# Performance work log

Hardware: AMD Instinct MI355X
Metric: run time of the kernel (lower is better)

Reference implementation:

```python
import jax, jax.numpy as jnp
import numpy as np
from math import sqrt

DIM = 256
NUM_HEADS = 4
GROUPS = 32  # min(256//4, 32)
EPS = 1e-6


def group_norm(x, gamma, beta, groups=GROUPS, eps=EPS):
    # x: (B, C, H, W); normalize per group over (C//G, H, W)
    B, C, H, W = x.shape
    xg = x.reshape(B, groups, C // groups, H, W)
    mu = jnp.mean(xg, axis=(2, 3, 4), keepdims=True)
    var = jnp.var(xg, axis=(2, 3, 4), keepdims=True)
    xn = ((xg - mu) * jax.lax.rsqrt(var + eps)).reshape(B, C, H, W)
    return xn * gamma[None, :, None, None] + beta[None, :, None, None]


def lin_on_channel(x, W, bias):
    # torch Linear on channel dim: W is (out, in)
    return jnp.einsum('bchw,oc->bohw', x, W) + bias[None, :, None, None]


def setup_inputs() -> dict:
    key = jax.random.key(0)
    ks = jax.random.split(key, 14)
    B, C, H, W = 16, DIM, 32, 32
    s = 1.0 / sqrt(DIM)
    return {
        'a': jax.random.normal(ks[0], (B, C, H, W), jnp.float32),
        'b': jax.random.normal(ks[1], (B, C, H, W), jnp.float32),
        'Wq': jax.random.normal(ks[2], (DIM, DIM), jnp.float32) * s,
        'bq': jnp.zeros((DIM,), jnp.float32),
        'Wk': jax.random.normal(ks[3], (DIM, DIM), jnp.float32) * s,
        'bk': jnp.zeros((DIM,), jnp.float32),
        'Wv': jax.random.normal(ks[4], (DIM, DIM), jnp.float32) * s,
        'bv': jnp.zeros((DIM,), jnp.float32),
        'Wp': jax.random.normal(ks[5], (DIM, DIM), jnp.float32) * s,
        'bp': jnp.zeros((DIM,), jnp.float32),
        'gnA_w': jnp.ones((DIM,), jnp.float32),
        'gnA_b': jnp.zeros((DIM,), jnp.float32),
        'gnB_w': jnp.ones((DIM,), jnp.float32),
        'gnB_b': jnp.zeros((DIM,), jnp.float32),
    }


def reference(a, b, Wq, bq, Wk, bk, Wv, bv, Wp, bp, gnA_w, gnA_b, gnB_w, gnB_b):
    B, C, H, W = a.shape
    _, _, H2, W2 = b.shape
    dh = DIM // NUM_HEADS
    skip_b = b
    an = group_norm(a, gnA_w, gnA_b)
    bn = group_norm(b, gnB_w, gnB_b)
    q = lin_on_channel(bn, Wq, bq).reshape(B, NUM_HEADS, dh, H2, W2)
    k = lin_on_channel(an, Wk, bk).reshape(B, NUM_HEADS, dh, H, W)
    # NOTE: value uses pre-posemb but post-groupnorm 'a' (same as an here)
    v = lin_on_channel(an, Wv, bv).reshape(B, NUM_HEADS, dh, H, W)
    scores = jnp.einsum('bhdxy,bhdij->bhxyij', q, k) / sqrt(DIM)
    attn = jax.nn.softmax(scores.reshape(B, NUM_HEADS, H2, W2, H * W), axis=-1)
    attn = attn.reshape(B, NUM_HEADS, H2, W2, H, W)
    h = jnp.einsum('bhxyij,bhdij->bhdxy', attn, v).reshape(B, DIM, H2, W2)
    h = lin_on_channel(h, Wp, bp)
    ret = skip_b + h
    return ret / sqrt(2.0)
```

## Files before the change

### kernel.cpp

```cpp
#include <hip/hip_runtime.h>
#include <hip/hip_bf16.h>

#define BSZ 16
#define CDIM 256
#define NPIX 1024
#define NH 4
#define DHD 64
#define EPSV 1e-6f
#define QSCALE 0.0625f
#define INV_SQRT2 0.70710678118654752440f

typedef __attribute__((ext_vector_type(4))) float f32x4;
typedef __attribute__((ext_vector_type(8))) __bf16 bf16x8;
typedef __attribute__((ext_vector_type(4))) __bf16 bf16x4;

#define OFF_WBF   0UL
#define OFF_STATS (512UL*1024)
#define OFF_ANT   (1024UL*1024)
#define OFF_BNT   (OFF_ANT + 8UL*1024*1024)
#define OFF_Q     (OFF_BNT + 8UL*1024*1024)
#define OFF_K     (OFF_Q   + 8UL*1024*1024)
#define OFF_V     (OFF_K   + 8UL*1024*1024)
#define OFF_H     (OFF_V   + 8UL*1024*1024)

__global__ __launch_bounds__(256) void prep_w(const float* __restrict__ Wq, const float* __restrict__ Wk,
                                              const float* __restrict__ Wv, const float* __restrict__ Wp,
                                              __bf16* __restrict__ out){
  int m = blockIdx.y;
  const float* src = (m==0)?Wq:(m==1)?Wk:(m==2)?Wv:Wp;
  float scale = (m==0)?QSCALE:1.0f;
  int idx = (blockIdx.x*256 + threadIdx.x)*4;
  float4 v = *(const float4*)(src + idx);
  bf16x4 o;
  o[0]=(__bf16)(v.x*scale); o[1]=(__bf16)(v.y*scale);
  o[2]=(__bf16)(v.z*scale); o[3]=(__bf16)(v.w*scale);
  *(bf16x4*)(out + m*65536 + idx) = o;
}

__global__ __launch_bounds__(256) void gn_stats(const float* __restrict__ xa, const float* __restrict__ xb,
                                                float2* __restrict__ stats){
  int bx = blockIdx.x;
  int t = bx >> 9; int rem = bx & 511; int bb = rem >> 5; int g = rem & 31;
  const float* src = (t ? xb : xa) + ((size_t)(bb*CDIM + g*8))*NPIX;
  float s = 0.f, ss = 0.f;
  for (int i = 0; i < 8; i++){
    float4 v = *(const float4*)(src + (threadIdx.x + 256*i)*4);
    s  += v.x+v.y+v.z+v.w;
    ss += v.x*v.x+v.y*v.y+v.z*v.z+v.w*v.w;
  }
  __shared__ float rs[256], rss[256];
  rs[threadIdx.x]=s; rss[threadIdx.x]=ss; __syncthreads();
  for (int st=128; st>0; st>>=1){
    if (threadIdx.x < st){ rs[threadIdx.x]+=rs[threadIdx.x+st]; rss[threadIdx.x]+=rss[threadIdx.x+st]; }
    __syncthreads();
  }
  if (threadIdx.x==0){
    float mean = rs[0]*(1.0f/8192.0f);
    float var  = rss[0]*(1.0f/8192.0f) - mean*mean;
    stats[(t*16+bb)*32+g] = make_float2(mean, rsqrtf(var + EPSV));
  }
}

__global__ __launch_bounds__(256) void norm_t(const float* __restrict__ xa, const float* __restrict__ xb,
                                              const float* __restrict__ gAw, const float* __restrict__ gAb,
                                              const float* __restrict__ gBw, const float* __restrict__ gBb,
                                              const float2* __restrict__ stats,
                                              __bf16* __restrict__ ant, __bf16* __restrict__ bnt){
  __shared__ __align__(16) __bf16 T[64][72];
  int t = blockIdx.z;
  const float* src = t ? xb : xa;
  const float* gw  = t ? gBw : gAw;
  const float* gb  = t ? gBb : gAb;
  __bf16* dst = t ? bnt : ant;
  int bb = blockIdx.y >> 2, cblk = blockIdx.y & 3;
  int p0 = blockIdx.x*64, c0 = cblk*64;
  int tid = threadIdx.x;
  int r16 = tid>>4, c4 = tid&15;
  for (int pass=0; pass<4; pass++){
    int cl = r16 + 16*pass;
    int c  = c0 + cl;
    float2 ms = stats[(t*16+bb)*32 + (c>>3)];
    float sc  = ms.y * gw[c];
    float off = gb[c] - ms.x*sc;
    float4 v = *(const float4*)(src + ((size_t)(bb*CDIM + c))*NPIX + p0 + c4*4);
    T[c4*4+0][cl] = (__bf16)(v.x*sc+off);
    T[c4*4+1][cl] = (__bf16)(v.y*sc+off);
    T[c4*4+2][cl] = (__bf16)(v.z*sc+off);
    T[c4*4+3][cl] = (__bf16)(v.w*sc+off);
  }
  __syncthreads();
  for (int pass=0; pass<2; pass++){
    int slot = tid + 256*pass;
    int pl = slot>>3, ch = slot&7;
    *(float4*)(dst + ((size_t)(bb*NPIX + p0 + pl))*CDIM + c0 + ch*8) = *(float4*)&T[pl][ch*8];
  }
}

__global__ __launch_bounds__(256) void gemm_k(const __bf16* __restrict__ A, const __bf16* __restrict__ Bm,
                                              const float* __restrict__ bias, float bias_scale,
                                              void* __restrict__ dst_, const float* __restrict__ skip,
                                              int mode){
  __shared__ __align__(16) __bf16 As[64][72], Bs[64][72];
  int tid = threadIdx.x;
  int m0 = blockIdx.y*64, n0 = blockIdx.x*64;
  int lane = tid & 63, wid = tid >> 6;
  int wm = (wid>>1)*32, wn = (wid&1)*32;
  int g = lane>>4, c = lane&15;
  f32x4 acc[2][2];
  #pragma unroll
  for (int i=0;i<2;i++)
    #pragma unroll
    for (int j=0;j<2;j++) acc[i][j] = (f32x4){0.f,0.f,0.f,0.f};

  for (int k0=0; k0<256; k0+=64){
    #pragma unroll
    for (int i=0;i<2;i++){
      int slot = tid + 256*i;
      int row = slot>>3, ch = slot&7;
      *(float4*)&As[row][ch*8] = *(const float4*)(A  + (size_t)(m0+row)*256 + k0 + ch*8);
      *(float4*)&Bs[row][ch*8] = *(const float4*)(Bm + (size_t)(n0+row)*256 + k0 + ch*8);
    }
    __syncthreads();
    #pragma unroll
    for (int ks=0; ks<2; ks++){
      bf16x8 af0 = *(bf16x8*)&As[wm +      c][ks*32 + g*8];
      bf16x8 af1 = *(bf16x8*)&As[wm + 16 + c][ks*32 + g*8];
      bf16x8 bf0 = *(bf16x8*)&Bs[wn +      c][ks*32 + g*8];
      bf16x8 bf1 = *(bf16x8*)&Bs[wn + 16 + c][ks*32 + g*8];
      acc[0][0] = __builtin_amdgcn_mfma_f32_16x16x32_bf16(af0, bf0, acc[0][0], 0,0,0);
      acc[0][1] = __builtin_amdgcn_mfma_f32_16x16x32_bf16(af0, bf1, acc[0][1], 0,0,0);
      acc[1][0] = __builtin_amdgcn_mfma_f32_16x16x32_bf16(af1, bf0, acc[1][0], 0,0,0);
      acc[1][1] = __builtin_amdgcn_mfma_f32_16x16x32_bf16(af1, bf1, acc[1][1], 0,0,0);
    }
    __syncthreads();
  }

  #pragma unroll
  for (int fm=0; fm<2; fm++){
    #pragma unroll
    for (int fn=0; fn<2; fn++){
      int m = m0 + wm + fm*16 + g*4;
      int n = n0 + wn + fn*16 + c;
      f32x4 v = acc[fm][fn];
      if (mode <= 1){
        int bb = n>>10, p = n&1023;
        int o = m, h = o>>6, d = o&63;
        bf16x4 pk;
        #pragma unroll
        for (int r=0;r<4;r++) pk[r] = (__bf16)(v[r] + bias[o+r]*bias_scale);
        *(bf16x4*)((__bf16*)dst_ + ((size_t)((bb*4+h)*1024 + p))*64 + d) = pk;
      } else if (mode == 2){
        int bb = m>>10, p = m&1023;
        int o = n, h = o>>6, d = o&63;
        float bv = bias[o];
        bf16x4 pk;
        #pragma unroll
        for (int r=0;r<4;r++) pk[r] = (__bf16)(v[r] + bv);
        *(bf16x4*)((__bf16*)dst_ + ((size_t)((bb*4+h)*64 + d))*1024 + p) = pk;
      } else {
        int bb = m>>10, p = m&1023;
        int o = n;
        float bv = bias[o];
        size_t addr = (size_t)(bb*256 + o)*1024 + p;
        float4 sk = *(const float4*)(skip + addr);
        float4 ov;
        ov.x = (sk.x + v[0] + bv)*INV_SQRT2;
        ov.y = (sk.y + v[1] + bv)*INV_SQRT2;
        ov.z = (sk.z + v[2] + bv)*INV_SQRT2;
        ov.w = (sk.w + v[3] + bv)*INV_SQRT2;
        *(float4*)((float*)dst_ + addr) = ov;
      }
    }
  }
}

__global__ __launch_bounds__(256) void attn_k(const __bf16* __restrict__ q, const __bf16* __restrict__ k,
                                              const __bf16* __restrict__ v, __bf16* __restrict__ hout){
  __shared__ __align__(16) __bf16 Kl[64][72], Vl[64][72], Pl[4][16][72];
  __shared__ float l_lds[4][16];
  int bh = blockIdx.y;
  int qblk = blockIdx.x;
  int tid = threadIdx.x, lane = tid&63, w = tid>>6;
  int g = lane>>4, c = lane&15;
  int bb = bh>>2, h = bh&3;
  const __bf16* qbase = q + (size_t)bh*NPIX*DHD;
  const __bf16* kbase = k + (size_t)bh*NPIX*DHD;
  const __bf16* vbase = v + (size_t)bh*DHD*NPIX;

  int qrow = qblk*64 + w*16 + c;
  bf16x8 qf0 = *(const bf16x8*)(qbase + (size_t)qrow*64 +      g*8);
  bf16x8 qf1 = *(const bf16x8*)(qbase + (size_t)qrow*64 + 32 + g*8);

  f32x4 oacc[4];
  #pragma unroll
  for (int i=0;i<4;i++) oacc[i] = (f32x4){0.f,0.f,0.f,0.f};
  float l0=0.f, l1=0.f, l2=0.f, l3=0.f;

  for (int kt=0; kt<16; kt++){
    #pragma unroll
    for (int i=0;i<2;i++){
      int slot = tid + 256*i;
      int row = slot>>3, ch = slot&7;
      *(float4*)&Kl[row][ch*8] = *(const float4*)(kbase + (size_t)(kt*64+row)*64 + ch*8);
      *(float4*)&Vl[row][ch*8] = *(const float4*)(vbase + (size_t)row*1024 + kt*64 + ch*8);
    }
    __syncthreads();
    f32x4 s[4];
    #pragma unroll
    for (int fn=0; fn<4; fn++){
      bf16x8 kb0 = *(bf16x8*)&Kl[fn*16 + c][     g*8];
      bf16x8 kb1 = *(bf16x8*)&Kl[fn*16 + c][32 + g*8];
      f32x4 z = (f32x4){0.f,0.f,0.f,0.f};
      z     = __builtin_amdgcn_mfma_f32_16x16x32_bf16(qf0, kb0, z, 0,0,0);
      s[fn] = __builtin_amdgcn_mfma_f32_16x16x32_bf16(qf1, kb1, z, 0,0,0);
    }
    #pragma unroll
    for (int fn=0; fn<4; fn++){
      float p0 = __expf(s[fn][0]); l0 += p0; Pl[w][g*4+0][fn*16+c] = (__bf16)p0;
      float p1 = __expf(s[fn][1]); l1 += p1; Pl[w][g*4+1][fn*16+c] = (__bf16)p1;
      float p2 = __expf(s[fn][2]); l2 += p2; Pl[w][g*4+2][fn*16+c] = (__bf16)p2;
      float p3 = __expf(s[fn][3]); l3 += p3; Pl[w][g*4+3][fn*16+c] = (__bf16)p3;
    }
    bf16x8 pb0 = *(bf16x8*)&Pl[w][c][     g*8];
    bf16x8 pb1 = *(bf16x8*)&Pl[w][c][32 + g*8];
    #pragma unroll
    for (int fm=0; fm<4; fm++){
      bf16x8 va0 = *(bf16x8*)&Vl[fm*16+c][     g*8];
      bf16x8 va1 = *(bf16x8*)&Vl[fm*16+c][32 + g*8];
      oacc[fm] = __builtin_amdgcn_mfma_f32_16x16x32_bf16(va0, pb0, oacc[fm], 0,0,0);
      oacc[fm] = __builtin_amdgcn_mfma_f32_16x16x32_bf16(va1, pb1, oacc[fm], 0,0,0);
    }
    __syncthreads();
  }

  l0 += __shfl_xor(l0,1); l0 += __shfl_xor(l0,2); l0 += __shfl_xor(l0,4); l0 += __shfl_xor(l0,8);
  l1 += __shfl_xor(l1,1); l1 += __shfl_xor(l1,2); l1 += __shfl_xor(l1,4); l1 += __shfl_xor(l1,8);
  l2 += __shfl_xor(l2,1); l2 += __shfl_xor(l2,2); l2 += __shfl_xor(l2,4); l2 += __shfl_xor(l2,8);
  l3 += __shfl_xor(l3,1); l3 += __shfl_xor(l3,2); l3 += __shfl_xor(l3,4); l3 += __shfl_xor(l3,8);
  float lv = (c==0)?l0:(c==1)?l1:(c==2)?l2:l3;
  if (c < 4) l_lds[w][g*4+c] = lv;
  __syncthreads();
  float linv = 1.0f / l_lds[w][c];

  int qg = qblk*64 + w*16 + c;
  #pragma unroll
  for (int fm=0; fm<4; fm++){
    bf16x4 pk;
    #pragma unroll
    for (int r=0;r<4;r++) pk[r] = (__bf16)(oacc[fm][r]*linv);
    *(bf16x4*)(hout + ((size_t)(bb*NPIX + qg))*CDIM + h*64 + fm*16 + g*4) = pk;
  }
}

extern "C" void kernel_launch(void* const* d_in, const int* in_sizes, int n_in,
                              void* d_out, int out_size, void* d_ws, size_t ws_size,
                              hipStream_t stream) {
  const float* xa  = (const float*)d_in[0];
  const float* xb  = (const float*)d_in[1];
  const float* Wq  = (const float*)d_in[2];
  const float* bq  = (const float*)d_in[3];
  const float* Wk  = (const float*)d_in[4];
  const float* bk  = (const float*)d_in[5];
  const float* Wv  = (const float*)d_in[6];
  const float* bv  = (const float*)d_in[7];
  const float* Wp  = (const float*)d_in[8];
  const float* bp  = (const float*)d_in[9];
  const float* gAw = (const float*)d_in[10];
  const float* gAb = (const float*)d_in[11];
  const float* gBw = (const float*)d_in[12];
  const float* gBb = (const float*)d_in[13];

  char* ws = (char*)d_ws;
  __bf16* wbf   = (__bf16*)(ws + OFF_WBF);
  float2* stats = (float2*)(ws + OFF_STATS);
  __bf16* ant   = (__bf16*)(ws + OFF_ANT);
  __bf16* bnt   = (__bf16*)(ws + OFF_BNT);
  __bf16* qws   = (__bf16*)(ws + OFF_Q);
  __bf16* kws   = (__bf16*)(ws + OFF_K);
  __bf16* vws   = (__bf16*)(ws + OFF_V);
  __bf16* hws   = (__bf16*)(ws + OFF_H);

  prep_w<<<dim3(64,4), 256, 0, stream>>>(Wq, Wk, Wv, Wp, wbf);
  gn_stats<<<1024, 256, 0, stream>>>(xa, xb, stats);
  norm_t<<<dim3(16,64,2), 256, 0, stream>>>(xa, xb, gAw, gAb, gBw, gBb, stats, ant, bnt);
  gemm_k<<<dim3(256,4), 256, 0, stream>>>(wbf,           bnt, bq, QSCALE, qws, nullptr, 0);
  gemm_k<<<dim3(256,4), 256, 0, stream>>>(wbf + 65536,   ant, bk, 1.0f,   kws, nullptr, 0);
  gemm_k<<<dim3(4,256), 256, 0, stream>>>(ant, wbf + 2*65536, bv, 1.0f,   vws, nullptr, 2);
  attn_k<<<dim3(16,64), 256, 0, stream>>>(qws, kws, vws, hws);
  gemm_k<<<dim3(4,256), 256, 0, stream>>>(hws, wbf + 3*65536, bp, 1.0f, d_out, xb, 3);
}
```

Measured before the change: 195.7 us.

## Merge Q/K GEMMs, enlarge GEMM tiles, prefetch global loads, remap blocks for XCD locality

Q and K projections are merged into one 128x128-tiled GEMM launch, and the V and output projections use a 128x64 tile, so there are fewer launches and more reuse per block. All GEMMs and the attention kernel now prefetch the next K-tile into registers while computing the current one. Block indices are remapped with an (i0&7) swizzle, LDS row padding changes from 72 to 76, and s_setprio is raised around the MFMA sections in attention. The costs are higher register pressure and possibly lower occupancy from the larger tiles.

Measured after the change: 259.7 us. +32.7%, slower.

```diff
diff --git a/kernel.cpp b/kernel.cpp
--- a/kernel.cpp
+++ b/kernel.cpp
@@ -96,78 +96,158 @@
   }
 }
 
-__global__ __launch_bounds__(256) void gemm_k(const __bf16* __restrict__ A, const __bf16* __restrict__ Bm,
-                                              const float* __restrict__ bias, float bias_scale,
-                                              void* __restrict__ dst_, const float* __restrict__ skip,
-                                              int mode){
-  __shared__ __align__(16) __bf16 As[64][72], Bs[64][72];
-  int tid = threadIdx.x;
-  int m0 = blockIdx.y*64, n0 = blockIdx.x*64;
-  int lane = tid & 63, wid = tid >> 6;
-  int wm = (wid>>1)*32, wn = (wid&1)*32;
-  int g = lane>>4, c = lane&15;
-  f32x4 acc[2][2];
-  #pragma unroll
-  for (int i=0;i<2;i++)
-    #pragma unroll
-    for (int j=0;j<2;j++) acc[i][j] = (f32x4){0.f,0.f,0.f,0.f};
-
-  for (int k0=0; k0<256; k0+=64){
-    #pragma unroll
-    for (int i=0;i<2;i++){
-      int slot = tid + 256*i;
-      int row = slot>>3, ch = slot&7;
-      *(float4*)&As[row][ch*8] = *(const float4*)(A  + (size_t)(m0+row)*256 + k0 + ch*8);
-      *(float4*)&Bs[row][ch*8] = *(const float4*)(Bm + (size_t)(n0+row)*256 + k0 + ch*8);
-    }
-    __syncthreads();
-    #pragma unroll
-    for (int ks=0; ks<2; ks++){
-      bf16x8 af0 = *(bf16x8*)&As[wm +      c][ks*32 + g*8];
-      bf16x8 af1 = *(bf16x8*)&As[wm + 16 + c][ks*32 + g*8];
-      bf16x8 bf0 = *(bf16x8*)&Bs[wn +      c][ks*32 + g*8];
-      bf16x8 bf1 = *(bf16x8*)&Bs[wn + 16 + c][ks*32 + g*8];
-      acc[0][0] = __builtin_amdgcn_mfma_f32_16x16x32_bf16(af0, bf0, acc[0][0], 0,0,0);
-      acc[0][1] = __builtin_amdgcn_mfma_f32_16x16x32_bf16(af0, bf1, acc[0][1], 0,0,0);
-      acc[1][0] = __builtin_amdgcn_mfma_f32_16x16x32_bf16(af1, bf0, acc[1][0], 0,0,0);
-      acc[1][1] = __builtin_amdgcn_mfma_f32_16x16x32_bf16(af1, bf1, acc[1][1], 0,0,0);
-    }
-    __syncthreads();
-  }
-
-  #pragma unroll
-  for (int fm=0; fm<2; fm++){
-    #pragma unroll
-    for (int fn=0; fn<2; fn++){
+__global__ __launch_bounds__(256) void gemm_qk(const __bf16* __restrict__ Wqk,
+    const __bf16* __restrict__ bnt, const __bf16* __restrict__ ant,
+    const float* __restrict__ bq, const float* __restrict__ bk,
+    __bf16* __restrict__ qws, __bf16* __restrict__ kws){
+  __shared__ __align__(16) __bf16 As[128][76], Bs[128][76];
+  int i0 = blockIdx.x;
+  int wg = (i0&7)*64 + (i0>>3);
+  int my = wg&3, nx = wg>>2;
+  int m0 = my*128, n0 = nx*128;
+  const __bf16* Bm = (my<2) ? bnt : ant;
+  int tid=threadIdx.x, lane=tid&63, wid=tid>>6;
+  int wm=(wid>>1)*64, wn=(wid&1)*64, g=lane>>4, c=lane&15;
+  f32x4 acc[4][4];
+  #pragma unroll
+  for (int i=0;i<4;i++)
+    #pragma unroll
+    for (int j=0;j<4;j++) acc[i][j]=(f32x4){0.f,0.f,0.f,0.f};
+  int row[4], ch[4];
+  #pragma unroll
+  for (int i=0;i<4;i++){ int slot=tid+256*i; row[i]=slot>>3; ch[i]=slot&7; }
+  float4 rA[4], rB[4];
+  #pragma unroll
+  for (int i=0;i<4;i++){
+    rA[i] = *(const float4*)(Wqk + (size_t)(m0+row[i])*256 + ch[i]*8);
+    rB[i] = *(const float4*)(Bm  + (size_t)(n0+row[i])*256 + ch[i]*8);
+  }
+  #pragma unroll
+  for (int t=0;t<4;t++){
+    #pragma unroll
+    for (int i=0;i<4;i++){
+      *(float4*)&As[row[i]][ch[i]*8] = rA[i];
+      *(float4*)&Bs[row[i]][ch[i]*8] = rB[i];
+    }
+    __syncthreads();
+    if (t<3){
+      int k0=(t+1)*64;
+      #pragma unroll
+      for (int i=0;i<4;i++){
+        rA[i] = *(const float4*)(Wqk + (size_t)(m0+row[i])*256 + k0 + ch[i]*8);
+        rB[i] = *(const float4*)(Bm  + (size_t)(n0+row[i])*256 + k0 + ch[i]*8);
+      }
+    }
+    #pragma unroll
+    for (int ks=0;ks<2;ks++){
+      bf16x8 af[4], bfr[4];
+      #pragma unroll
+      for (int i=0;i<4;i++) af[i]  = *(bf16x8*)&As[wm+i*16+c][ks*32+g*8];
+      #pragma unroll
+      for (int j=0;j<4;j++) bfr[j] = *(bf16x8*)&Bs[wn+j*16+c][ks*32+g*8];
+      #pragma unroll
+      for (int i=0;i<4;i++)
+        #pragma unroll
+        for (int j=0;j<4;j++)
+          acc[i][j] = __builtin_amdgcn_mfma_f32_16x16x32_bf16(af[i], bfr[j], acc[i][j],0,0,0);
+    }
+    __syncthreads();
+  }
+  const float* bias = (my<2)? bq : bk;
+  float bscale = (my<2)? QSCALE : 1.0f;
+  __bf16* dst = (my<2)? qws : kws;
+  int mbase = (my<2)? m0 : (m0-256);
+  #pragma unroll
+  for (int fm=0;fm<4;fm++){
+    #pragma unroll
+    for (int fn=0;fn<4;fn++){
+      int o = mbase + wm + fm*16 + g*4;
+      int n = n0 + wn + fn*16 + c;
+      int bb=n>>10, p=n&1023;
+      f32x4 v = acc[fm][fn];
+      bf16x4 pk;
+      #pragma unroll
+      for (int r=0;r<4;r++) pk[r] = (__bf16)(v[r] + bias[o+r]*bscale);
+      *(bf16x4*)(dst + ((size_t)((bb*4+(o>>6))*1024 + p))*64 + (o&63)) = pk;
+    }
+  }
+}
+
+__global__ __launch_bounds__(256) void gemm_sw(const __bf16* __restrict__ A,
+    const __bf16* __restrict__ Wn, const float* __restrict__ bias,
+    void* __restrict__ dst_, const float* __restrict__ skip, int mode){
+  __shared__ __align__(16) __bf16 As[128][76], Bs[64][76];
+  int i0 = blockIdx.x;
+  int wg = (i0&7)*64 + (i0>>3);
+  int ny = wg&3, mx = wg>>2;
+  int m0 = mx*128, n0 = ny*64;
+  int tid=threadIdx.x, lane=tid&63, wid=tid>>6;
+  int wm=(wid>>1)*64, wn=(wid&1)*32, g=lane>>4, c=lane&15;
+  f32x4 acc[4][2];
+  #pragma unroll
+  for (int i=0;i<4;i++)
+    #pragma unroll
+    for (int j=0;j<2;j++) acc[i][j]=(f32x4){0.f,0.f,0.f,0.f};
+  int rowA[4], chA[4], rowB[2], chB[2];
+  #pragma unroll
+  for (int i=0;i<4;i++){ int slot=tid+256*i; rowA[i]=slot>>3; chA[i]=slot&7; }
+  #pragma unroll
+  for (int i=0;i<2;i++){ int slot=tid+256*i; rowB[i]=slot>>3; chB[i]=slot&7; }
+  float4 rA[4], rB[2];
+  #pragma unroll
+  for (int i=0;i<4;i++) rA[i] = *(const float4*)(A  + (size_t)(m0+rowA[i])*256 + chA[i]*8);
+  #pragma unroll
+  for (int i=0;i<2;i++) rB[i] = *(const float4*)(Wn + (size_t)(n0+rowB[i])*256 + chB[i]*8);
+  #pragma unroll
+  for (int t=0;t<4;t++){
+    #pragma unroll
+    for (int i=0;i<4;i++) *(float4*)&As[rowA[i]][chA[i]*8] = rA[i];
+    #pragma unroll
+    for (int i=0;i<2;i++) *(float4*)&Bs[rowB[i]][chB[i]*8] = rB[i];
+    __syncthreads();
+    if (t<3){
+      int k0=(t+1)*64;
+      #pragma unroll
+      for (int i=0;i<4;i++) rA[i] = *(const float4*)(A  + (size_t)(m0+rowA[i])*256 + k0 + chA[i]*8);
+      #pragma unroll
+      for (int i=0;i<2;i++) rB[i] = *(const float4*)(Wn + (size_t)(n0+rowB[i])*256 + k0 + chB[i]*8);
+    }
+    #pragma unroll
+    for (int ks=0;ks<2;ks++){
+      bf16x8 af[4], bfr[2];
+      #pragma unroll
+      for (int i=0;i<4;i++) af[i]  = *(bf16x8*)&As[wm+i*16+c][ks*32+g*8];
+      #pragma unroll
+      for (int j=0;j<2;j++) bfr[j] = *(bf16x8*)&Bs[wn+j*16+c][ks*32+g*8];
+      #pragma unroll
+      for (int i=0;i<4;i++)
+        #pragma unroll
+        for (int j=0;j<2;j++)
+          acc[i][j] = __builtin_amdgcn_mfma_f32_16x16x32_bf16(af[i], bfr[j], acc[i][j],0,0,0);
+    }
+    __syncthreads();
+  }
+  #pragma unroll
+  for (int fm=0;fm<4;fm++){
+    #pragma unroll
+    for (int fn=0;fn<2;fn++){
       int m = m0 + wm + fm*16 + g*4;
       int n = n0 + wn + fn*16 + c;
+      int bb=m>>10, p=m&1023;
       f32x4 v = acc[fm][fn];
-      if (mode <= 1){
-        int bb = n>>10, p = n&1023;
-        int o = m, h = o>>6, d = o&63;
-        bf16x4 pk;
-        #pragma unroll
-        for (int r=0;r<4;r++) pk[r] = (__bf16)(v[r] + bias[o+r]*bias_scale);
-        *(bf16x4*)((__bf16*)dst_ + ((size_t)((bb*4+h)*1024 + p))*64 + d) = pk;
-      } else if (mode == 2){
-        int bb = m>>10, p = m&1023;
-        int o = n, h = o>>6, d = o&63;
-        float bv = bias[o];
+      if (mode==0){
+        float bv = bias[n];
         bf16x4 pk;
         #pragma unroll
         for (int r=0;r<4;r++) pk[r] = (__bf16)(v[r] + bv);
-        *(bf16x4*)((__bf16*)dst_ + ((size_t)((bb*4+h)*64 + d))*1024 + p) = pk;
+        *(bf16x4*)((__bf16*)dst_ + ((size_t)((bb*4+(n>>6))*64 + (n&63)))*1024 + p) = pk;
       } else {
-        int bb = m>>10, p = m&1023;
-        int o = n;
-        float bv = bias[o];
-        size_t addr = (size_t)(bb*256 + o)*1024 + p;
+        float bv = bias[n];
+        size_t addr = (size_t)(bb*256 + n)*1024 + p;
         float4 sk = *(const float4*)(skip + addr);
         float4 ov;
-        ov.x = (sk.x + v[0] + bv)*INV_SQRT2;
-        ov.y = (sk.y + v[1] + bv)*INV_SQRT2;
-        ov.z = (sk.z + v[2] + bv)*INV_SQRT2;
-        ov.w = (sk.w + v[3] + bv)*INV_SQRT2;
+        ov.x=(sk.x+v[0]+bv)*INV_SQRT2; ov.y=(sk.y+v[1]+bv)*INV_SQRT2;
+        ov.z=(sk.z+v[2]+bv)*INV_SQRT2; ov.w=(sk.w+v[3]+bv)*INV_SQRT2;
         *(float4*)((float*)dst_ + addr) = ov;
       }
     }
@@ -176,10 +256,11 @@
 
 __global__ __launch_bounds__(256) void attn_k(const __bf16* __restrict__ q, const __bf16* __restrict__ k,
                                               const __bf16* __restrict__ v, __bf16* __restrict__ hout){
-  __shared__ __align__(16) __bf16 Kl[64][72], Vl[64][72], Pl[4][16][72];
+  __shared__ __align__(16) __bf16 Kl[64][76], Vl[64][76], Pl[4][16][76];
   __shared__ float l_lds[4][16];
-  int bh = blockIdx.y;
-  int qblk = blockIdx.x;
+  int i0 = blockIdx.x;
+  int wg = (i0&7)*128 + (i0>>3);
+  int bh = wg>>4, qblk = wg&15;
   int tid = threadIdx.x, lane = tid&63, w = tid>>6;
   int g = lane>>4, c = lane&15;
   int bb = bh>>2, h = bh&3;
@@ -196,16 +277,32 @@
   for (int i=0;i<4;i++) oacc[i] = (f32x4){0.f,0.f,0.f,0.f};
   float l0=0.f, l1=0.f, l2=0.f, l3=0.f;
 
+  int srow[2], sch[2];
+  #pragma unroll
+  for (int i=0;i<2;i++){ int slot=tid+256*i; srow[i]=slot>>3; sch[i]=slot&7; }
+  float4 rK[2], rV[2];
+  #pragma unroll
+  for (int i=0;i<2;i++){
+    rK[i] = *(const float4*)(kbase + (size_t)srow[i]*64 + sch[i]*8);
+    rV[i] = *(const float4*)(vbase + (size_t)srow[i]*1024 + sch[i]*8);
+  }
+
   for (int kt=0; kt<16; kt++){
     #pragma unroll
     for (int i=0;i<2;i++){
-      int slot = tid + 256*i;
-      int row = slot>>3, ch = slot&7;
-      *(float4*)&Kl[row][ch*8] = *(const float4*)(kbase + (size_t)(kt*64+row)*64 + ch*8);
-      *(float4*)&Vl[row][ch*8] = *(const float4*)(vbase + (size_t)row*1024 + kt*64 + ch*8);
-    }
-    __syncthreads();
+      *(float4*)&Kl[srow[i]][sch[i]*8] = rK[i];
+      *(float4*)&Vl[srow[i]][sch[i]*8] = rV[i];
+    }
+    __syncthreads();
+    if (kt<15){
+      #pragma unroll
+      for (int i=0;i<2;i++){
+        rK[i] = *(const float4*)(kbase + (size_t)((kt+1)*64+srow[i])*64 + sch[i]*8);
+        rV[i] = *(const float4*)(vbase + (size_t)srow[i]*1024 + (kt+1)*64 + sch[i]*8);
+      }
+    }
     f32x4 s[4];
+    __builtin_amdgcn_s_setprio(1);
     #pragma unroll
     for (int fn=0; fn<4; fn++){
       bf16x8 kb0 = *(bf16x8*)&Kl[fn*16 + c][     g*8];
@@ -214,6 +311,7 @@
       z     = __builtin_amdgcn_mfma_f32_16x16x32_bf16(qf0, kb0, z, 0,0,0);
       s[fn] = __builtin_amdgcn_mfma_f32_16x16x32_bf16(qf1, kb1, z, 0,0,0);
     }
+    __builtin_amdgcn_s_setprio(0);
     #pragma unroll
     for (int fn=0; fn<4; fn++){
       float p0 = __expf(s[fn][0]); l0 += p0; Pl[w][g*4+0][fn*16+c] = (__bf16)p0;
@@ -223,6 +321,7 @@
     }
     bf16x8 pb0 = *(bf16x8*)&Pl[w][c][     g*8];
     bf16x8 pb1 = *(bf16x8*)&Pl[w][c][32 + g*8];
+    __builtin_amdgcn_s_setprio(1);
     #pragma unroll
     for (int fm=0; fm<4; fm++){
       bf16x8 va0 = *(bf16x8*)&Vl[fm*16+c][     g*8];
@@ -230,6 +329,7 @@
       oacc[fm] = __builtin_amdgcn_mfma_f32_16x16x32_bf16(va0, pb0, oacc[fm], 0,0,0);
       oacc[fm] = __builtin_amdgcn_mfma_f32_16x16x32_bf16(va1, pb1, oacc[fm], 0,0,0);
     }
+    __builtin_amdgcn_s_setprio(0);
     __syncthreads();
   }
 
@@ -283,9 +383,8 @@
   prep_w<<<dim3(64,4), 256, 0, stream>>>(Wq, Wk, Wv, Wp, wbf);
   gn_stats<<<1024, 256, 0, stream>>>(xa, xb, stats);
   norm_t<<<dim3(16,64,2), 256, 0, stream>>>(xa, xb, gAw, gAb, gBw, gBb, stats, ant, bnt);
-  gemm_k<<<dim3(256,4), 256, 0, stream>>>(wbf,           bnt, bq, QSCALE, qws, nullptr, 0);
-  gemm_k<<<dim3(256,4), 256, 0, stream>>>(wbf + 65536,   ant, bk, 1.0f,   kws, nullptr, 0);
-  gemm_k<<<dim3(4,256), 256, 0, stream>>>(ant, wbf + 2*65536, bv, 1.0f,   vws, nullptr, 2);
-  attn_k<<<dim3(16,64), 256, 0, stream>>>(qws, kws, vws, hws);
-  gemm_k<<<dim3(4,256), 256, 0, stream>>>(hws, wbf + 3*65536, bp, 1.0f, d_out, xb, 3);
-}
+  gemm_qk<<<512, 256, 0, stream>>>(wbf, bnt, ant, bq, bk, qws, kws);
+  gemm_sw<<<512, 256, 0, stream>>>(ant, wbf + 2*65536, bv, vws, nullptr, 0);
+  attn_k<<<1024, 256, 0, stream>>>(qws, kws, vws, hws);
+  gemm_sw<<<512, 256, 0, stream>>>(hws, wbf + 3*65536, bp, d_out, xb, 1);
+}
```
